# Optimization experiments

Hardware: AMD Instinct MI355X
Metric: run time of the kernel (lower is better)

Reference implementation:

```python
import jax, jax.numpy as jnp
import numpy as np

EPS = 1e-5
HEADS = 8
SR = 4


def bn(x, gamma, beta, mean, var):
    # BatchNorm in inference form; channel axis = 1
    shape = (1, -1) + (1,) * (x.ndim - 2)
    inv = gamma.reshape(shape) / jnp.sqrt(var.reshape(shape) + EPS)
    return (x - mean.reshape(shape)) * inv + beta.reshape(shape)


def setup_inputs() -> dict:
    key = jax.random.key(0)
    ks = jax.random.split(key, 8)
    B, C, H, W = 2, 256, 128, 128
    N = H * W
    conv1d_std = np.sqrt(2.0 / C)            # fan_out = 1*C
    conv2d_std = np.sqrt(2.0 / (SR * SR * C))  # fan_out = sr*sr*C
    return {
        "x": jax.random.normal(ks[0], (B, C, N), dtype=jnp.float32),
        "w_q": jax.random.normal(ks[1], (C, C), dtype=jnp.float32) * conv1d_std,
        "w_k": jax.random.normal(ks[2], (C, C), dtype=jnp.float32) * conv1d_std,
        "w_sr": jax.random.normal(ks[3], (C, C, SR, SR), dtype=jnp.float32) * conv2d_std,
        "sr_gamma": jnp.ones((C,), jnp.float32),
        "sr_beta": jnp.zeros((C,), jnp.float32),
        "sr_mean": jnp.zeros((C,), jnp.float32),
        "sr_var": jnp.ones((C,), jnp.float32),
        "w_proj": jax.random.normal(ks[4], (C, C), dtype=jnp.float32) * conv1d_std,
        "proj_gamma": jnp.ones((C,), jnp.float32),
        "proj_beta": jnp.zeros((C,), jnp.float32),
        "proj_mean": jnp.zeros((C,), jnp.float32),
        "proj_var": jnp.ones((C,), jnp.float32),
        "H": 128,
        "W": 128,
    }


def reference(x, w_q, w_k, w_sr, sr_gamma, sr_beta, sr_mean, sr_var,
              w_proj, proj_gamma, proj_beta, proj_mean, proj_var, H, W):
    B, C, N = x.shape
    hd = C // HEADS
    scale = hd ** -0.5
    # q: Conv1d(k=1) == channel matmul -> (B, heads, N, hd)
    q = jnp.einsum('oc,bcn->bon', w_q, x).reshape(B, HEADS, hd, N).transpose(0, 1, 3, 2)
    # spatial reduction: Conv2d(k=SR, s=SR) as patch-reshape + einsum, then BN
    xp = x.reshape(B, C, H // SR, SR, W // SR, SR)
    xr = jnp.einsum('bchpwq,ocpq->bohw', xp, w_sr).reshape(B, C, (H // SR) * (W // SR))
    xr = bn(xr, sr_gamma, sr_beta, sr_mean, sr_var)
    # k: (B, heads, hd, N_kv)
    k = jnp.einsum('oc,bcm->bom', w_k, xr).reshape(B, HEADS, hd, -1)
    # scores (B, heads, N, N_kv) -> max over kv
    scores = jnp.einsum('bhnd,bhdm->bhnm', q, k) * scale
    attn = scores.max(axis=-1)                # (B, heads, N)
    # v = mean-pooled x, identical per head -> matmul collapses to sum over heads
    v = x.mean(axis=-1)                       # (B, C)
    out = jnp.einsum('bhn,bc->bcn', attn, v)  # (B, C, N)
    out = jnp.einsum('oc,bcn->bon', w_proj, out)
    return bn(out, proj_gamma, proj_beta, proj_mean, proj_var)
```

## Files before the change

### kernel.cpp

```cpp
#include <hip/hip_runtime.h>
#include <hip/hip_bf16.h>
#include <math.h>

#define EPSF 1e-5f
#define SCALE 0.17677669529663687f

typedef __bf16 bf16x8 __attribute__((ext_vector_type(8)));
typedef __bf16 bf16x4 __attribute__((ext_vector_type(4)));
typedef float f32x4 __attribute__((ext_vector_type(4)));


__global__ __launch_bounds__(256) void k_wprep(const float* __restrict__ wq,
                                               const float* __restrict__ wk,
                                               const float* __restrict__ wsr,
                                               __bf16* __restrict__ wqf,
                                               __bf16* __restrict__ wkb,
                                               __bf16* __restrict__ wsrf,
                                               float* __restrict__ v,
                                               float* __restrict__ ssg) {
    int bi = blockIdx.x, t = threadIdx.x;
    if (bi >= 576) {
        int e = (bi - 576) * 256 + t;
        *(float4*)&ssg[e << 2] = make_float4(0.f, 0.f, 0.f, 0.f);
        return;
    }
    if (bi < 32) {
        if (bi == 0) { v[t] = 0.f; v[256 + t] = 0.f; }
        int tt = bi * 256 + t;
        int o = tt >> 5, chunk = tt & 31;
        float4 v0 = *(const float4*)&wq[o * 256 + (chunk << 3)];
        float4 v1 = *(const float4*)&wq[o * 256 + (chunk << 3) + 4];
        bf16x8 p;
        p[0] = (__bf16)v0.x; p[1] = (__bf16)v0.y; p[2] = (__bf16)v0.z; p[3] = (__bf16)v0.w;
        p[4] = (__bf16)v1.x; p[5] = (__bf16)v1.y; p[6] = (__bf16)v1.z; p[7] = (__bf16)v1.w;
        int cc = chunk >> 2, quad = chunk & 3;
        *(bf16x8*)&wqf[(((((o >> 4) << 3) + cc) << 6) + (quad << 4) + (o & 15)) << 3] = p;
    } else if (bi < 64) {
        int e = (bi - 32) * 256 + t;
        float4 v0 = *(const float4*)&wk[e << 3];
        float4 v1 = *(const float4*)&wk[(e << 3) + 4];
        bf16x8 p;
        p[0] = (__bf16)(v0.x * SCALE); p[1] = (__bf16)(v0.y * SCALE);
        p[2] = (__bf16)(v0.z * SCALE); p[3] = (__bf16)(v0.w * SCALE);
        p[4] = (__bf16)(v1.x * SCALE); p[5] = (__bf16)(v1.y * SCALE);
        p[6] = (__bf16)(v1.z * SCALE); p[7] = (__bf16)(v1.w * SCALE);
        *(bf16x8*)&wkb[e << 3] = p;
    } else {
        int tt = (bi - 64) * 256 + t;
        int o = tt >> 9, chunk = tt & 511;
        float4 v0 = *(const float4*)&wsr[o * 4096 + (chunk << 3)];
        float4 v1 = *(const float4*)&wsr[o * 4096 + (chunk << 3) + 4];
        bf16x8 p;
        p[0] = (__bf16)v0.x; p[1] = (__bf16)v0.y; p[2] = (__bf16)v0.z; p[3] = (__bf16)v0.w;
        p[4] = (__bf16)v1.x; p[5] = (__bf16)v1.y; p[6] = (__bf16)v1.z; p[7] = (__bf16)v1.w;
        int cc = chunk >> 2, quad = chunk & 3;
        *(bf16x8*)&wsrf[(((((o >> 4) << 7) + cc) << 6) + (quad << 4) + (o & 15)) << 3] = p;
    }
}

__global__ __launch_bounds__(256) void k_stage(const float* __restrict__ x,
                                               __bf16* __restrict__ Pbf,
                                               __bf16* __restrict__ xTf,
                                               float* __restrict__ v) {
    int t = threadIdx.x, bid0 = blockIdx.x;
    if (bid0 < 512) {
        __shared__ float csum[32];
        int bid = bid0;
        int b = bid >> 8, hm = (bid >> 3) & 31, ccg = bid & 7;
        int wm = t >> 3, c8 = t & 7;
        if (t < 32) csum[t] = 0.f;
        __syncthreads();
        const int mtile = (hm << 1) + (wm >> 4);
        const int ln = wm & 15;
#pragma unroll
        for (int cci = 0; cci < 4; ++cci) {
            int c = (ccg << 5) + (cci << 3) + c8;
            const float* src = x + ((size_t)(b * 256 + c) << 14) + (hm << 9) + (wm << 2);
            bf16x8 o0, o1;
            float s = 0.f;
#pragma unroll
            for (int p = 0; p < 2; ++p) {
                float4 vv = *(const float4*)&src[p << 7];
                s += vv.x + vv.y + vv.z + vv.w;
                o0[p * 4 + 0] = (__bf16)vv.x; o0[p * 4 + 1] = (__bf16)vv.y;
                o0[p * 4 + 2] = (__bf16)vv.z; o0[p * 4 + 3] = (__bf16)vv.w;
            }
#pragma unroll
            for (int p = 0; p < 2; ++p) {
                float4 vv = *(const float4*)&src[(p + 2) << 7];
                s += vv.x + vv.y + vv.z + vv.w;
                o1[p * 4 + 0] = (__bf16)vv.x; o1[p * 4 + 1] = (__bf16)vv.y;
                o1[p * 4 + 2] = (__bf16)vv.z; o1[p * 4 + 3] = (__bf16)vv.w;
            }
            size_t d0 = (((((size_t)(b * 64 + mtile) << 7) + (c >> 1)) << 6) +
                         (((c & 1) << 1) << 4) + ln) << 3;
            *(bf16x8*)&Pbf[d0] = o0;
            *(bf16x8*)&Pbf[d0 + 128] = o1;
            atomicAdd(&csum[(cci << 3) + c8], s);
        }
        __syncthreads();
        if (t < 32) atomicAdd(&v[b * 256 + (ccg << 5) + t], csum[t]);
    } else {
        __shared__ float ts[32 * 68];
        int bid = bid0 - 512;
        int b = bid >> 8, n0 = (bid & 255) << 6;
        const int nl = t >> 2;
        const int ch = (t & 3) << 3;
        const int n = n0 + nl;
        const int ntile = n >> 4, ln = n & 15, quad = ch >> 3;
        const int cl = t >> 3;
        const int n8 = (t & 7) << 3;
        for (int s8 = 0; s8 < 8; ++s8) {
            int c0 = s8 << 5;
            __syncthreads();
            {
                const float* src = &x[((size_t)(b * 256 + c0 + cl) << 14) + n0 + n8];
                *(float4*)&ts[cl * 68 + n8] = *(const float4*)&src[0];
                *(float4*)&ts[cl * 68 + n8 + 4] = *(const float4*)&src[4];
            }
            __syncthreads();
            bf16x8 p;
#pragma unroll
            for (int j = 0; j < 8; ++j) p[j] = (__bf16)ts[(ch + j) * 68 + nl];
            *(bf16x8*)&xTf[(((((size_t)(b * 1024 + ntile) << 3) + s8) << 6) +
                            (quad << 4) + ln) << 3] = p;
        }
    }
}

__global__ __launch_bounds__(256) void k_conv1f(const __bf16* __restrict__ Pbf,
                                                const __bf16* __restrict__ wsrf,
                                                const float* __restrict__ sg,
                                                const float* __restrict__ sb,
                                                const float* __restrict__ smn,
                                                const float* __restrict__ svar,
                                                __bf16* __restrict__ xrb) {
    const int t = threadIdx.x, bid = blockIdx.x;
    const int b = bid & 1, mt = (bid >> 1) & 63, og = bid >> 7;
    const int w = t >> 6, lane = t & 63, ln = lane & 15, quad = lane >> 4;
    f32x4 acc = (f32x4){0.f, 0.f, 0.f, 0.f};
    const __bf16* pa = Pbf + ((size_t)(b * 64 + mt) << 16) + (lane << 3);
    const __bf16* pbm = wsrf + ((size_t)(og * 4 + w) << 16) + (lane << 3);
#pragma unroll 8
    for (int cc = 0; cc < 128; ++cc) {
        bf16x8 af = *(const bf16x8*)&pa[cc << 9];
        bf16x8 bf = *(const bf16x8*)&pbm[cc << 9];
        acc = __builtin_amdgcn_mfma_f32_16x16x32_bf16(af, bf, acc, 0, 0, 0);
    }
    const int o = (og << 6) + (w << 4) + ln;
    float inv = sg[o] / sqrtf(svar[o] + EPSF);
    float mn = smn[o], bt = sb[o];
#pragma unroll
    for (int r = 0; r < 4; ++r) {
        int m = (mt << 4) + (quad << 2) + r;
        xrb[(((size_t)b << 10) + m) * 256 + o] = (__bf16)((acc[r] - mn) * inv + bt);
    }
}

__global__ __launch_bounds__(256) void k_kmat2(const __bf16* __restrict__ xrb,
                                               const __bf16* __restrict__ wkb,
                                               __bf16* __restrict__ kkbh,
                                               const float* __restrict__ v,
                                               const float* __restrict__ wproj,
                                               const float* __restrict__ pg,
                                               const float* __restrict__ pb,
                                               const float* __restrict__ pm,
                                               const float* __restrict__ pvar,
                                               float* __restrict__ A,
                                               float* __restrict__ B0) {
    const int t = threadIdx.x, bid = blockIdx.x;
    if (bid >= 128) {
        __shared__ float vl[256];
        int b = bid - 128;
        vl[t] = v[b * 256 + t] * (1.0f / 16384.0f);
        __syncthreads();
        const float* wr = wproj + t * 256;
        float s = 0.f;
#pragma unroll 8
        for (int c = 0; c < 256; c += 4) {
            float4 w4 = *(const float4*)&wr[c];
            s += w4.x * vl[c] + w4.y * vl[c + 1] + w4.z * vl[c + 2] + w4.w * vl[c + 3];
        }
        float inv = pg[t] / sqrtf(pvar[t] + EPSF);
        A[b * 256 + t] = s * inv;
        if (b == 0) B0[t] = pb[t] - pm[t] * inv;
        return;
    }
    const int b = bid >> 6, mt = bid & 63;
    const int w = t >> 6, lane = t & 63, ln = lane & 15, quad = lane >> 4;
    f32x4 acc[4];
#pragma unroll
    for (int ot = 0; ot < 4; ++ot) acc[ot] = (f32x4){0.f, 0.f, 0.f, 0.f};
    const __bf16* pa = xrb + ((((size_t)b << 10) + (mt << 4) + ln) << 8) + (quad << 3);
    const __bf16* pbm = wkb + (((w << 6) + ln) << 8) + (quad << 3);
#pragma unroll
    for (int cc = 0; cc < 8; ++cc) {
        const int cb = cc << 5;
        bf16x8 af = *(const bf16x8*)&pa[cb];
        bf16x8 bfr[4];
#pragma unroll
        for (int ot = 0; ot < 4; ++ot) bfr[ot] = *(const bf16x8*)&pbm[(ot << 12) + cb];
#pragma unroll
        for (int ot = 0; ot < 4; ++ot)
            acc[ot] = __builtin_amdgcn_mfma_f32_16x16x32_bf16(af, bfr[ot], acc[ot], 0, 0, 0);
    }
#pragma unroll
    for (int ot = 0; ot < 4; ++ot)
#pragma unroll
        for (int r = 0; r < 4; ++r) {
            int m = (mt << 4) + (quad << 2) + r;
            int h = (w << 1) + (ot >> 1);
            int d = ((ot & 1) << 4) + ln;
            kkbh[(((size_t)(b * 8 + h)) << 15) + (m << 5) + d] = (__bf16)acc[ot][r];
        }
}

__global__ __launch_bounds__(256) void k_scores2(const __bf16* __restrict__ xTf,
                                                 const __bf16* __restrict__ wqf,
                                                 const __bf16* __restrict__ kkbh,
                                                 float* __restrict__ ssg) {
    __shared__ __align__(16) __bf16 qs[64 * 72];
    __shared__ float smax[512];
    const int t = threadIdx.x;
    const int w = t >> 6;
    const int lane = t & 63;
    const int ln = lane & 15;
    const int quad = lane >> 4;
    const int bx = blockIdx.x;
    const int hp = bx & 3;
    const int n0 = ((bx >> 2) & 255) << 6;
    const int b = bx >> 10;

    f32x4 acc[4];
#pragma unroll
    for (int ot = 0; ot < 4; ++ot) acc[ot] = (f32x4){0.f, 0.f, 0.f, 0.f};
    const __bf16* pa = xTf + ((size_t)(b * 1024 + (n0 >> 4) + w) << 12) + (lane << 3);
    const __bf16* pbm = wqf + ((size_t)(hp << 2) << 12) + (lane << 3);
#pragma unroll 2
    for (int cc = 0; cc < 8; ++cc) {
        const int cb = cc << 9;
        bf16x8 af = *(const bf16x8*)&pa[cb];
        bf16x8 bfr[4];
#pragma unroll
        for (int ot = 0; ot < 4; ++ot) bfr[ot] = *(const bf16x8*)&pbm[(ot << 12) + cb];
#pragma unroll
        for (int ot = 0; ot < 4; ++ot)
            acc[ot] = __builtin_amdgcn_mfma_f32_16x16x32_bf16(af, bfr[ot], acc[ot], 0, 0, 0);
    }
#pragma unroll
    for (int ot = 0; ot < 4; ++ot)
#pragma unroll
        for (int r = 0; r < 4; ++r)
            qs[((w << 4) + (quad << 2) + r) * 72 + (ot << 4) + ln] = (__bf16)acc[ot][r];
    __syncthreads();

    const f32x4 zf = {0.f, 0.f, 0.f, 0.f};
#pragma unroll
    for (int hl = 0; hl < 2; ++hl) {
        const int h = (hp << 1) + hl;
        bf16x8 qb[4];
#pragma unroll
        for (int nt = 0; nt < 4; ++nt)
            qb[nt] = *(const bf16x8*)&qs[((nt << 4) + ln) * 72 + (hl << 5) + (quad << 3)];
        const __bf16* kb_base = kkbh + ((size_t)(b * 8 + h) << 15) + (ln << 5) + (quad << 3);
        bf16x8 kb[16];
#pragma unroll
        for (int i = 0; i < 16; ++i)
            kb[i] = *(const bf16x8*)&kb_base[((w << 8) + (i << 4)) << 5];
        float rmx[4] = {-INFINITY, -INFINITY, -INFINITY, -INFINITY};
#pragma unroll
        for (int i = 0; i < 16; ++i)
#pragma unroll
            for (int nt = 0; nt < 4; ++nt) {
                f32x4 d = __builtin_amdgcn_mfma_f32_16x16x32_bf16(kb[i], qb[nt], zf, 0, 0, 0);
                float t1 = fmaxf(fmaxf(d[0], d[1]), d[2]);
                rmx[nt] = fmaxf(fmaxf(t1, d[3]), rmx[nt]);
            }
#pragma unroll
        for (int nt = 0; nt < 4; ++nt) {
            rmx[nt] = fmaxf(rmx[nt], __shfl_xor(rmx[nt], 16, 64));
            rmx[nt] = fmaxf(rmx[nt], __shfl_xor(rmx[nt], 32, 64));
        }
        if (lane < 16) {
#pragma unroll
            for (int nt = 0; nt < 4; ++nt)
                smax[(w << 7) + (hl << 6) + (nt << 4) + lane] = rmx[nt];
        }
    }
    __syncthreads();
    if (t < 64) {
        float s0 = fmaxf(fmaxf(smax[t], smax[128 + t]), fmaxf(smax[256 + t], smax[384 + t]));
        float s1 = fmaxf(fmaxf(smax[64 + t], smax[192 + t]),
                         fmaxf(smax[320 + t], smax[448 + t]));
        atomicAdd(&ssg[(b << 14) + n0 + t], s0 + s1);
    }
}

__global__ __launch_bounds__(256) void k_epi(const float* __restrict__ ssg,
                                             const float* __restrict__ A,
                                             const float* __restrict__ B0,
                                             float* __restrict__ out) {
    __shared__ float ss[64], sA[256], sB[256];
    const int t = threadIdx.x, bid = blockIdx.x;
    const int b = bid >> 8, n0 = (bid & 255) << 6;
    if (t < 64) ss[t] = ssg[(b << 14) + n0 + t];
    sA[t] = A[b * 256 + t];
    sB[t] = B0[t];
    __syncthreads();
#pragma unroll
    for (int i = 0; i < 16; ++i) {
        int e = t + (i << 8);
        int c = e >> 4, n4 = (e & 15) << 2;
        float4 s4 = *(const float4*)&ss[n4];
        float a = sA[c], bb = sB[c];
        float4 o4 = make_float4(fmaf(a, s4.x, bb), fmaf(a, s4.y, bb),
                                fmaf(a, s4.z, bb), fmaf(a, s4.w, bb));
        *(float4*)&out[((size_t)(b * 256 + c) << 14) + n0 + n4] = o4;
    }
}

extern "C" void kernel_launch(void* const* d_in, const int* in_sizes, int n_in,
                              void* d_out, int out_size, void* d_ws, size_t ws_size,
                              hipStream_t stream) {
    const float* x    = (const float*)d_in[0];
    const float* wq   = (const float*)d_in[1];
    const float* wk   = (const float*)d_in[2];
    const float* wsr  = (const float*)d_in[3];
    const float* sg   = (const float*)d_in[4];
    const float* sb   = (const float*)d_in[5];
    const float* smn  = (const float*)d_in[6];
    const float* svr  = (const float*)d_in[7];
    const float* wproj= (const float*)d_in[8];
    const float* pg   = (const float*)d_in[9];
    const float* pb   = (const float*)d_in[10];
    const float* pm   = (const float*)d_in[11];
    const float* pvr  = (const float*)d_in[12];
    float* out = (float*)d_out;

    char* W = (char*)d_ws;
    float*  w_v   = (float*) (W + 0);
    float*  w_A   = (float*) (W + 4096);
    float*  w_B0  = (float*) (W + 8192);
    float*  w_ssg = (float*) (W + 12288);
    __bf16* w_wqf = (__bf16*)(W + 147456);
    __bf16* w_wkb = (__bf16*)(W + 278528);
    __bf16* w_wsrf= (__bf16*)(W + 409600);
    __bf16* w_xrb = (__bf16*)(W + 2506752);
    __bf16* w_kkbh= (__bf16*)(W + 3031040);
    __bf16* w_Pbf = (__bf16*)(W + 4079616);
    __bf16* w_xTf = (__bf16*)(W + 20856832);

    k_wprep<<<608, 256, 0, stream>>>(wq, wk, wsr, w_wqf, w_wkb, w_wsrf, w_v, w_ssg);
    k_stage<<<1024, 256, 0, stream>>>(x, w_Pbf, w_xTf, w_v);
    k_conv1f<<<512, 256, 0, stream>>>(w_Pbf, w_wsrf, sg, sb, smn, svr, w_xrb);
    k_kmat2<<<130, 256, 0, stream>>>(w_xrb, w_wkb, w_kkbh, w_v, wproj, pg, pb, pm, pvr,
                                     w_A, w_B0);
    k_scores2<<<2048, 256, 0, stream>>>(w_xTf, w_wqf, w_kkbh, w_ssg);
    k_epi<<<512, 256, 0, stream>>>(w_ssg, w_A, w_B0, out);
}
```

Measured before the change: 190.4 us.

## Merge kernels: fold patch staging into prep, conv into stage, epilogue into scores

Reorganizes the six-launch pipeline into four launches. Patch staging for the conv moves into the weight-prep kernel, the spatial-reduction conv runs alongside the transpose staging (which now also computes the channel sums), and the final epilogue is fused into the scores kernel via a per-chunk atomic counter where the last of four head blocks writes the output. Also adds s_setprio around the MFMA loop. This removes launch gaps and one pass over ssg, at the cost of atomic counter traffic, fences and tail work in the last-finishing block.

```diff
diff --git a/kernel.cpp b/kernel.cpp
--- a/kernel.cpp
+++ b/kernel.cpp
@@ -6,20 +6,53 @@
 #define SCALE 0.17677669529663687f
 
 typedef __bf16 bf16x8 __attribute__((ext_vector_type(8)));
-typedef __bf16 bf16x4 __attribute__((ext_vector_type(4)));
 typedef float f32x4 __attribute__((ext_vector_type(4)));
 
 
-__global__ __launch_bounds__(256) void k_wprep(const float* __restrict__ wq,
-                                               const float* __restrict__ wk,
-                                               const float* __restrict__ wsr,
-                                               __bf16* __restrict__ wqf,
-                                               __bf16* __restrict__ wkb,
-                                               __bf16* __restrict__ wsrf,
-                                               float* __restrict__ v,
-                                               float* __restrict__ ssg) {
-    int bi = blockIdx.x, t = threadIdx.x;
+__global__ __launch_bounds__(256) void k_prep(const float* __restrict__ wq,
+                                              const float* __restrict__ wk,
+                                              const float* __restrict__ wsr,
+                                              const float* __restrict__ x,
+                                              __bf16* __restrict__ wqf,
+                                              __bf16* __restrict__ wkb,
+                                              __bf16* __restrict__ wsrf,
+                                              __bf16* __restrict__ Pbf,
+                                              float* __restrict__ v,
+                                              float* __restrict__ ssg,
+                                              int* __restrict__ cnt) {
+    const int bi = blockIdx.x, t = threadIdx.x;
+    if (bi >= 608) {
+        const int bid = bi - 608;
+        const int b = bid >> 8, hm = (bid >> 3) & 31, ccg = bid & 7;
+        const int wm = t >> 3, c8 = t & 7;
+        const int mtile = (hm << 1) + (wm >> 4);
+        const int ln = wm & 15;
+#pragma unroll
+        for (int cci = 0; cci < 4; ++cci) {
+            const int c = (ccg << 5) + (cci << 3) + c8;
+            const float* src = x + ((size_t)(b * 256 + c) << 14) + (hm << 9) + (wm << 2);
+            bf16x8 o0, o1;
+#pragma unroll
+            for (int p = 0; p < 2; ++p) {
+                float4 vv = *(const float4*)&src[p << 7];
+                o0[p * 4 + 0] = (__bf16)vv.x; o0[p * 4 + 1] = (__bf16)vv.y;
+                o0[p * 4 + 2] = (__bf16)vv.z; o0[p * 4 + 3] = (__bf16)vv.w;
+            }
+#pragma unroll
+            for (int p = 0; p < 2; ++p) {
+                float4 vv = *(const float4*)&src[(p + 2) << 7];
+                o1[p * 4 + 0] = (__bf16)vv.x; o1[p * 4 + 1] = (__bf16)vv.y;
+                o1[p * 4 + 2] = (__bf16)vv.z; o1[p * 4 + 3] = (__bf16)vv.w;
+            }
+            size_t d0 = (((((size_t)(b * 64 + mtile) << 7) + (c >> 1)) << 6) +
+                         (((c & 1) << 1) << 4) + ln) << 3;
+            *(bf16x8*)&Pbf[d0] = o0;
+            *(bf16x8*)&Pbf[d0 + 128] = o1;
+        }
+        return;
+    }
     if (bi >= 576) {
+        if (bi == 576 && t < 128) *(int4*)&cnt[t << 2] = make_int4(0, 0, 0, 0);
         int e = (bi - 576) * 256 + t;
         *(float4*)&ssg[e << 2] = make_float4(0.f, 0.f, 0.f, 0.f);
         return;
@@ -58,65 +91,60 @@
     }
 }
 
-__global__ __launch_bounds__(256) void k_stage(const float* __restrict__ x,
-                                               __bf16* __restrict__ Pbf,
-                                               __bf16* __restrict__ xTf,
-                                               float* __restrict__ v) {
-    int t = threadIdx.x, bid0 = blockIdx.x;
+__global__ __launch_bounds__(256) void k_cx(const __bf16* __restrict__ Pbf,
+                                            const __bf16* __restrict__ wsrf,
+                                            const float* __restrict__ sg,
+                                            const float* __restrict__ sb,
+                                            const float* __restrict__ smn,
+                                            const float* __restrict__ svar,
+                                            __bf16* __restrict__ xrb,
+                                            const float* __restrict__ x,
+                                            __bf16* __restrict__ xTf,
+                                            float* __restrict__ v) {
+    const int t = threadIdx.x, bid0 = blockIdx.x;
     if (bid0 < 512) {
-        __shared__ float csum[32];
-        int bid = bid0;
-        int b = bid >> 8, hm = (bid >> 3) & 31, ccg = bid & 7;
-        int wm = t >> 3, c8 = t & 7;
-        if (t < 32) csum[t] = 0.f;
-        __syncthreads();
-        const int mtile = (hm << 1) + (wm >> 4);
-        const int ln = wm & 15;
-#pragma unroll
-        for (int cci = 0; cci < 4; ++cci) {
-            int c = (ccg << 5) + (cci << 3) + c8;
-            const float* src = x + ((size_t)(b * 256 + c) << 14) + (hm << 9) + (wm << 2);
-            bf16x8 o0, o1;
-            float s = 0.f;
-#pragma unroll
-            for (int p = 0; p < 2; ++p) {
-                float4 vv = *(const float4*)&src[p << 7];
-                s += vv.x + vv.y + vv.z + vv.w;
-                o0[p * 4 + 0] = (__bf16)vv.x; o0[p * 4 + 1] = (__bf16)vv.y;
-                o0[p * 4 + 2] = (__bf16)vv.z; o0[p * 4 + 3] = (__bf16)vv.w;
-            }
-#pragma unroll
-            for (int p = 0; p < 2; ++p) {
-                float4 vv = *(const float4*)&src[(p + 2) << 7];
-                s += vv.x + vv.y + vv.z + vv.w;
-                o1[p * 4 + 0] = (__bf16)vv.x; o1[p * 4 + 1] = (__bf16)vv.y;
-                o1[p * 4 + 2] = (__bf16)vv.z; o1[p * 4 + 3] = (__bf16)vv.w;
-            }
-            size_t d0 = (((((size_t)(b * 64 + mtile) << 7) + (c >> 1)) << 6) +
-                         (((c & 1) << 1) << 4) + ln) << 3;
-            *(bf16x8*)&Pbf[d0] = o0;
-            *(bf16x8*)&Pbf[d0 + 128] = o1;
-            atomicAdd(&csum[(cci << 3) + c8], s);
-        }
-        __syncthreads();
-        if (t < 32) atomicAdd(&v[b * 256 + (ccg << 5) + t], csum[t]);
+        const int b = bid0 & 1, mt = (bid0 >> 1) & 63, og = bid0 >> 7;
+        const int w = t >> 6, lane = t & 63, ln = lane & 15, quad = lane >> 4;
+        f32x4 acc = (f32x4){0.f, 0.f, 0.f, 0.f};
+        const __bf16* pa = Pbf + ((size_t)(b * 64 + mt) << 16) + (lane << 3);
+        const __bf16* pbm = wsrf + ((size_t)(og * 4 + w) << 16) + (lane << 3);
+#pragma unroll 8
+        for (int cc = 0; cc < 128; ++cc) {
+            bf16x8 af = *(const bf16x8*)&pa[cc << 9];
+            bf16x8 bf = *(const bf16x8*)&pbm[cc << 9];
+            acc = __builtin_amdgcn_mfma_f32_16x16x32_bf16(af, bf, acc, 0, 0, 0);
+        }
+        const int o = (og << 6) + (w << 4) + ln;
+        float inv = sg[o] / sqrtf(svar[o] + EPSF);
+        float mn = smn[o], bt = sb[o];
+#pragma unroll
+        for (int r = 0; r < 4; ++r) {
+            int m = (mt << 4) + (quad << 2) + r;
+            xrb[(((size_t)b << 10) + m) * 256 + o] = (__bf16)((acc[r] - mn) * inv + bt);
+        }
     } else {
         __shared__ float ts[32 * 68];
-        int bid = bid0 - 512;
-        int b = bid >> 8, n0 = (bid & 255) << 6;
+        __shared__ float sv[256];
+        const int bid = bid0 - 512;
+        const int b = bid >> 8, n0 = (bid & 255) << 6;
         const int nl = t >> 2;
         const int ch = (t & 3) << 3;
         const int n = n0 + nl;
         const int ntile = n >> 4, ln = n & 15, quad = ch >> 3;
         const int cl = t >> 3;
         const int n8 = (t & 7) << 3;
+        sv[t] = 0.f;
         for (int s8 = 0; s8 < 8; ++s8) {
-            int c0 = s8 << 5;
+            const int c0 = s8 << 5;
             __syncthreads();
             {
                 const float* src = &x[((size_t)(b * 256 + c0 + cl) << 14) + n0 + n8];
-                *(float4*)&ts[cl * 68 + n8] = *(const float4*)&src[0];
-                *(float4*)&ts[cl * 68 + n8 + 4] = *(const float4*)&src[4];
+                float4 a0 = *(const float4*)&src[0];
+                float4 a1 = *(const float4*)&src[4];
+                *(float4*)&ts[cl * 68 + n8] = a0;
+                *(float4*)&ts[cl * 68 + n8 + 4] = a1;
+                atomicAdd(&sv[c0 + cl],
+                          a0.x + a0.y + a0.z + a0.w + a1.x + a1.y + a1.z + a1.w);
             }
             __syncthreads();
             bf16x8 p;
@@ -125,35 +153,8 @@
             *(bf16x8*)&xTf[(((((size_t)(b * 1024 + ntile) << 3) + s8) << 6) +
                             (quad << 4) + ln) << 3] = p;
         }
-    }
-}
-
-__global__ __launch_bounds__(256) void k_conv1f(const __bf16* __restrict__ Pbf,
-                                                const __bf16* __restrict__ wsrf,
-                                                const float* __restrict__ sg,
-                                                const float* __restrict__ sb,
-                                                const float* __restrict__ smn,
-                                                const float* __restrict__ svar,
-                                                __bf16* __restrict__ xrb) {
-    const int t = threadIdx.x, bid = blockIdx.x;
-    const int b = bid & 1, mt = (bid >> 1) & 63, og = bid >> 7;
-    const int w = t >> 6, lane = t & 63, ln = lane & 15, quad = lane >> 4;
-    f32x4 acc = (f32x4){0.f, 0.f, 0.f, 0.f};
-    const __bf16* pa = Pbf + ((size_t)(b * 64 + mt) << 16) + (lane << 3);
-    const __bf16* pbm = wsrf + ((size_t)(og * 4 + w) << 16) + (lane << 3);
-#pragma unroll 8
-    for (int cc = 0; cc < 128; ++cc) {
-        bf16x8 af = *(const bf16x8*)&pa[cc << 9];
-        bf16x8 bf = *(const bf16x8*)&pbm[cc << 9];
-        acc = __builtin_amdgcn_mfma_f32_16x16x32_bf16(af, bf, acc, 0, 0, 0);
-    }
-    const int o = (og << 6) + (w << 4) + ln;
-    float inv = sg[o] / sqrtf(svar[o] + EPSF);
-    float mn = smn[o], bt = sb[o];
-#pragma unroll
-    for (int r = 0; r < 4; ++r) {
-        int m = (mt << 4) + (quad << 2) + r;
-        xrb[(((size_t)b << 10) + m) * 256 + o] = (__bf16)((acc[r] - mn) * inv + bt);
+        __syncthreads();
+        atomicAdd(&v[b * 256 + t], sv[t]);
     }
 }
 
@@ -215,12 +216,17 @@
         }
 }
 
-__global__ __launch_bounds__(256) void k_scores2(const __bf16* __restrict__ xTf,
-                                                 const __bf16* __restrict__ wqf,
-                                                 const __bf16* __restrict__ kkbh,
-                                                 float* __restrict__ ssg) {
+__global__ __launch_bounds__(256) void k_sc(const __bf16* __restrict__ xTf,
+                                            const __bf16* __restrict__ wqf,
+                                            const __bf16* __restrict__ kkbh,
+                                            float* __restrict__ ssg,
+                                            int* __restrict__ cnt,
+                                            const float* __restrict__ A,
+                                            const float* __restrict__ B0,
+                                            float* __restrict__ out) {
     __shared__ __align__(16) __bf16 qs[64 * 72];
     __shared__ float smax[512];
+    __shared__ int sdone;
     const int t = threadIdx.x;
     const int w = t >> 6;
     const int lane = t & 63;
@@ -228,7 +234,8 @@
     const int quad = lane >> 4;
     const int bx = blockIdx.x;
     const int hp = bx & 3;
-    const int n0 = ((bx >> 2) & 255) << 6;
+    const int nch = (bx >> 2) & 255;
+    const int n0 = nch << 6;
     const int b = bx >> 10;
 
     f32x4 acc[4];
@@ -268,6 +275,7 @@
         for (int i = 0; i < 16; ++i)
             kb[i] = *(const bf16x8*)&kb_base[((w << 8) + (i << 4)) << 5];
         float rmx[4] = {-INFINITY, -INFINITY, -INFINITY, -INFINITY};
+        __builtin_amdgcn_s_setprio(1);
 #pragma unroll
         for (int i = 0; i < 16; ++i)
 #pragma unroll
@@ -276,6 +284,7 @@
                 float t1 = fmaxf(fmaxf(d[0], d[1]), d[2]);
                 rmx[nt] = fmaxf(fmaxf(t1, d[3]), rmx[nt]);
             }
+        __builtin_amdgcn_s_setprio(0);
 #pragma unroll
         for (int nt = 0; nt < 4; ++nt) {
             rmx[nt] = fmaxf(rmx[nt], __shfl_xor(rmx[nt], 16, 64));
@@ -294,16 +303,20 @@
                          fmaxf(smax[320 + t], smax[448 + t]));
         atomicAdd(&ssg[(b << 14) + n0 + t], s0 + s1);
     }
-}
-
-__global__ __launch_bounds__(256) void k_epi(const float* __restrict__ ssg,
-                                             const float* __restrict__ A,
-                                             const float* __restrict__ B0,
-                                             float* __restrict__ out) {
-    __shared__ float ss[64], sA[256], sB[256];
-    const int t = threadIdx.x, bid = blockIdx.x;
-    const int b = bid >> 8, n0 = (bid & 255) << 6;
-    if (t < 64) ss[t] = ssg[(b << 14) + n0 + t];
+    __threadfence();
+    __syncthreads();
+    if (t == 0)
+        sdone = (__hip_atomic_fetch_add(&cnt[(b << 8) + nch], 1,
+                                        __ATOMIC_ACQ_REL,
+                                        __HIP_MEMORY_SCOPE_AGENT) == 3);
+    __syncthreads();
+    if (!sdone) return;
+    float* sA = (float*)qs;
+    float* sB = sA + 256;
+    float* sS = sA + 512;
+    if (t < 64)
+        sS[t] = __hip_atomic_load(&ssg[(b << 14) + n0 + t], __ATOMIC_RELAXED,
+                                  __HIP_MEMORY_SCOPE_AGENT);
     sA[t] = A[b * 256 + t];
     sB[t] = B0[t];
     __syncthreads();
@@ -311,7 +324,7 @@
     for (int i = 0; i < 16; ++i) {
         int e = t + (i << 8);
         int c = e >> 4, n4 = (e & 15) << 2;
-        float4 s4 = *(const float4*)&ss[n4];
+        float4 s4 = *(const float4*)&sS[n4];
         float a = sA[c], bb = sB[c];
         float4 o4 = make_float4(fmaf(a, s4.x, bb), fmaf(a, s4.y, bb),
                                 fmaf(a, s4.z, bb), fmaf(a, s4.w, bb));
@@ -342,6 +355,7 @@
     float*  w_A   = (float*) (W + 4096);
     float*  w_B0  = (float*) (W + 8192);
     float*  w_ssg = (float*) (W + 12288);
+    int*    w_cnt = (int*)   (W + 143360);
     __bf16* w_wqf = (__bf16*)(W + 147456);
     __bf16* w_wkb = (__bf16*)(W + 278528);
     __bf16* w_wsrf= (__bf16*)(W + 409600);
@@ -350,11 +364,11 @@
     __bf16* w_Pbf = (__bf16*)(W + 4079616);
     __bf16* w_xTf = (__bf16*)(W + 20856832);
 
-    k_wprep<<<608, 256, 0, stream>>>(wq, wk, wsr, w_wqf, w_wkb, w_wsrf, w_v, w_ssg);
-    k_stage<<<1024, 256, 0, stream>>>(x, w_Pbf, w_xTf, w_v);
-    k_conv1f<<<512, 256, 0, stream>>>(w_Pbf, w_wsrf, sg, sb, smn, svr, w_xrb);
+    k_prep<<<1120, 256, 0, stream>>>(wq, wk, wsr, x, w_wqf, w_wkb, w_wsrf, w_Pbf,
+                                     w_v, w_ssg, w_cnt);
+    k_cx<<<1024, 256, 0, stream>>>(w_Pbf, w_wsrf, sg, sb, smn, svr, w_xrb,
+                                   x, w_xTf, w_v);
     k_kmat2<<<130, 256, 0, stream>>>(w_xrb, w_wkb, w_kkbh, w_v, wproj, pg, pb, pm, pvr,
                                      w_A, w_B0);
-    k_scores2<<<2048, 256, 0, stream>>>(w_xTf, w_wqf, w_kkbh, w_ssg);
-    k_epi<<<512, 256, 0, stream>>>(w_ssg, w_A, w_B0, out);
-}
+    k_sc<<<2048, 256, 0, stream>>>(w_xTf, w_wqf, w_kkbh, w_ssg, w_cnt, w_A, w_B0, out);
+}
```

After: 485.1 us. 2.55x slower.
